# Performance work log

Hardware: AMD Instinct MI355X
Metric: run time of the kernel (lower is better)

The kernel has to match this reference:

```python
import jax, jax.numpy as jnp
import numpy as np

D_MODEL = 1024
N_HEADS = 16
D_HEAD = 64
N_CTX = 2048
ROTARY_DIM = 64
ROTARY_BASE = 10000.0
ATTN_SCALE = 8.0
IGNORE = -100000.0


def _sin_cos(seq_len):
    # rotary_adjacent_pairs=False -> freq repeated as '(2 d)'
    pos = jnp.arange(seq_len, dtype=jnp.float32)
    dim = jnp.arange(ROTARY_DIM // 2, dtype=jnp.float32)
    freq = ROTARY_BASE ** (dim / (ROTARY_DIM / 2))
    freq = jnp.concatenate([freq, freq])  # (2 d)
    angles = pos[:, None] / freq[None, :]  # [S, rotary_dim]
    return jnp.sin(angles), jnp.cos(angles)


def _apply_rotary(x, sin, cos):
    # x: [B, S, H, d_head]; rotary_dim == d_head here, pass-through part is empty
    x_rot = x[..., :ROTARY_DIM]
    x_pass = x[..., ROTARY_DIM:]
    n = ROTARY_DIM // 2
    x_flip = jnp.concatenate([-x_rot[..., n:], x_rot[..., :n]], axis=-1)
    x_rotated = x_rot * cos[None, :, None, :] + x_flip * sin[None, :, None, :]
    return jnp.concatenate([x_rotated, x_pass], axis=-1)


def setup_inputs() -> dict:
    key = jax.random.key(0)
    ks = jax.random.split(key, 12)
    B, S = 1, 2048
    f = lambda k, shp, s=1.0: jax.random.normal(k, shp, dtype=jnp.float32) * s
    return {
        "xq": f(ks[0], (B, S, N_HEADS, D_MODEL)),
        "xk": f(ks[1], (B, S, N_HEADS, D_MODEL)),
        "xv": f(ks[2], (B, S, N_HEADS, D_MODEL)),
        "W_Q": f(ks[3], (N_HEADS, D_MODEL, D_HEAD), 0.02),
        "b_Q": jnp.zeros((N_HEADS, D_HEAD), jnp.float32),
        "W_K": f(ks[4], (N_HEADS, D_MODEL, D_HEAD), 0.02),
        "b_K": jnp.zeros((N_HEADS, D_HEAD), jnp.float32),
        "W_V": f(ks[5], (N_HEADS, D_MODEL, D_HEAD), 0.02),
        "b_V": jnp.zeros((N_HEADS, D_HEAD), jnp.float32),
        "W_O": f(ks[6], (N_HEADS, D_HEAD, D_MODEL), 0.02),
        "b_O": jnp.zeros((D_MODEL,), jnp.float32),
    }


def reference(xq, xk, xv, W_Q, b_Q, W_K, b_K, W_V, b_V, W_O, b_O):
    S = xq.shape[1]
    sin, cos = _sin_cos(S)
    # per-head QKV projections: [B,S,H,dm] x [H,dm,dh] -> [B,S,H,dh]
    q = jnp.einsum('bsnd,nde->bsne', xq, W_Q) + b_Q
    k = jnp.einsum('bsnd,nde->bsne', xk, W_K) + b_K
    v = jnp.einsum('bsnd,nde->bsne', xv, W_V) + b_V
    q = _apply_rotary(q, sin, cos)
    k = _apply_rotary(k, sin, cos)
    # attention scores [B,H,Q,K]
    scores = jnp.einsum('bqne,bkne->bnqk', q, k) / ATTN_SCALE
    causal = jnp.triu(jnp.ones((S, S), dtype=bool), k=1)
    scores = jnp.where(causal[None, None], IGNORE, scores)
    pattern = jax.nn.softmax(scores, axis=-1)
    z = jnp.einsum('bnqk,bkne->bqne', pattern, v)
    # NOTE: faithful to source — head dim is NOT summed; b_O divided by n_heads
    attn_out = jnp.einsum('bqne,ned->bqnd', z, W_O) + b_O / N_HEADS
    return attn_out
```

## Files before the change

### kernel.cpp

```cpp
#include <hip/hip_runtime.h>
#include <hip/hip_bf16.h>
#include <stdint.h>
#include <math.h>

typedef __bf16 bf16_t;
typedef __bf16 bf16x8 __attribute__((ext_vector_type(8)));
typedef __bf16 bf16x4 __attribute__((ext_vector_type(4)));
typedef float  f32x4  __attribute__((ext_vector_type(4)));

#define S_CTX 2048
#define NH    16
#define DM    1024
#define DH    64

#define WS_WT   0
#define WS_WOT  (3*1048576)
#define WS_Q    (4*1048576)
#define WS_K    (WS_Q  + 2097152)
#define WS_VT   (WS_K  + 2097152)
#define WS_Z    (WS_VT + 2097152)

__global__ __launch_bounds__(256) void transpose_w(const float* __restrict__ wq,
                                                   const float* __restrict__ wk,
                                                   const float* __restrict__ wv,
                                                   const float* __restrict__ wo,
                                                   bf16_t* __restrict__ ws) {
  __shared__ bf16_t tl[64 * 68];
  int m = blockIdx.z, h = blockIdx.y, t = blockIdx.x, tid = threadIdx.x;
  const float* in; bf16_t* out; int R, C, r0, c0;
  if (m < 3) { in = (m == 0) ? wq : (m == 1) ? wk : wv; out = ws + m * 1048576;
               R = 1024; C = 64; r0 = t * 64; c0 = 0; }
  else       { in = wo; out = ws + WS_WOT; R = 64; C = 1024; r0 = 0; c0 = t * 64; }
  in  += h * 65536;
  out += h * 65536;
#pragma unroll
  for (int i = 0; i < 4; i++) {
    int idx = tid + i * 256;
    int r = idx >> 4, c = (idx & 15) << 2;
    float4 v = *reinterpret_cast<const float4*>(in + (r0 + r) * C + c0 + c);
    bf16x4 b;
    b[0] = (bf16_t)v.x; b[1] = (bf16_t)v.y; b[2] = (bf16_t)v.z; b[3] = (bf16_t)v.w;
    *reinterpret_cast<bf16x4*>(tl + r * 68 + c) = b;
  }
  __syncthreads();
#pragma unroll
  for (int i = 0; i < 2; i++) {
    int oc = (tid >> 3) + i * 32, ok = (tid & 7) << 3;
    bf16x8 v;
#pragma unroll
    for (int j = 0; j < 8; j++) v[j] = tl[(ok + j) * 68 + oc];
    *reinterpret_cast<bf16x8*>(out + (c0 + oc) * R + r0 + ok) = v;
  }
}

__global__ __launch_bounds__(256) void qkv_proj(const float* __restrict__ xq,
                                                const float* __restrict__ xk,
                                                const float* __restrict__ xv,
                                                const float* __restrict__ bq,
                                                const float* __restrict__ bk,
                                                const float* __restrict__ bv,
                                                bf16_t* __restrict__ ws) {
  __shared__ bf16_t Al[128 * 136];
  __shared__ bf16_t Bl[64 * 136];
  int st = blockIdx.x, h = blockIdx.y, m = blockIdx.z;
  int tid = threadIdx.x, w = tid >> 6, lane = tid & 63, quad = lane >> 4, l15 = lane & 15;
  const float*  in   = (m == 0) ? xq : (m == 1) ? xk : xv;
  const bf16_t* wT   = ws + m * 1048576 + h * 65536;
  const float*  bias = (m == 0) ? bq : (m == 1) ? bk : bv;
  int s0 = st * 128;
  const float* Ab = in + (s0 * 16 + h) * 1024;

  f32x4 acc[2][4];
#pragma unroll
  for (int rt = 0; rt < 2; rt++)
#pragma unroll
    for (int t = 0; t < 4; t++) acc[rt][t] = (f32x4){0.f, 0.f, 0.f, 0.f};

  for (int k0 = 0; k0 < 1024; k0 += 128) {
#pragma unroll
    for (int i = 0; i < 8; i++) {
      int g = tid + i * 256;
      int r = g >> 4, cg = g & 15;
      const float* p = Ab + r * 16384 + k0 + cg * 8;
      float4 v0 = *reinterpret_cast<const float4*>(p);
      float4 v1 = *reinterpret_cast<const float4*>(p + 4);
      bf16x8 b;
      b[0] = (bf16_t)v0.x; b[1] = (bf16_t)v0.y; b[2] = (bf16_t)v0.z; b[3] = (bf16_t)v0.w;
      b[4] = (bf16_t)v1.x; b[5] = (bf16_t)v1.y; b[6] = (bf16_t)v1.z; b[7] = (bf16_t)v1.w;
      *reinterpret_cast<bf16x8*>(Al + r * 136 + cg * 8) = b;
    }
#pragma unroll
    for (int i = 0; i < 4; i++) {
      int g = tid + i * 256;
      int r = g >> 4, cg = g & 15;
      *reinterpret_cast<uint4*>(Bl + r * 136 + cg * 8) =
          *reinterpret_cast<const uint4*>(wT + r * 1024 + k0 + cg * 8);
    }
    __syncthreads();
#pragma unroll
    for (int ks = 0; ks < 4; ks++) {
      bf16x8 a0 = *reinterpret_cast<const bf16x8*>(Al + (w * 32 + l15) * 136 + ks * 32 + quad * 8);
      bf16x8 a1 = *reinterpret_cast<const bf16x8*>(Al + (w * 32 + 16 + l15) * 136 + ks * 32 + quad * 8);
#pragma unroll
      for (int t = 0; t < 4; t++) {
        bf16x8 bb = *reinterpret_cast<const bf16x8*>(Bl + (t * 16 + l15) * 136 + ks * 32 + quad * 8);
        acc[0][t] = __builtin_amdgcn_mfma_f32_16x16x32_bf16(a0, bb, acc[0][t], 0, 0, 0);
        acc[1][t] = __builtin_amdgcn_mfma_f32_16x16x32_bf16(a1, bb, acc[1][t], 0, 0, 0);
      }
    }
    __syncthreads();
  }
#pragma unroll
  for (int t = 0; t < 4; t++) {
    float bval = bias[h * 64 + t * 16 + l15];
#pragma unroll
    for (int rt = 0; rt < 2; rt++)
#pragma unroll
      for (int r = 0; r < 4; r++) acc[rt][t][r] += bval;
  }

  if (m < 2) {
    bf16_t* outp = ws + ((m == 0) ? WS_Q : WS_K) + h * (2048 * 64);
#pragma unroll
    for (int t = 0; t < 2; t++) {
      int c_lo = t * 16 + l15;
      float freq = powf(10000.0f, (float)c_lo * (1.0f / 32.0f));
#pragma unroll
      for (int rt = 0; rt < 2; rt++)
#pragma unroll
        for (int r = 0; r < 4; r++) {
          int s = s0 + w * 32 + rt * 16 + quad * 4 + r;
          float ang = (float)s / freq;
          float sv = sinf(ang), cv = cosf(ang);
          float xl = acc[rt][t][r], xh = acc[rt][t + 2][r];
          acc[rt][t][r]     = xl * cv - xh * sv;
          acc[rt][t + 2][r] = xh * cv + xl * sv;
        }
    }
#pragma unroll
    for (int rt = 0; rt < 2; rt++)
#pragma unroll
      for (int t = 0; t < 4; t++)
#pragma unroll
        for (int r = 0; r < 4; r++) {
          int s = s0 + w * 32 + rt * 16 + quad * 4 + r;
          outp[s * 64 + t * 16 + l15] = (bf16_t)acc[rt][t][r];
        }
  } else {
    bf16_t* outp = ws + WS_VT + h * (64 * 2048);
#pragma unroll
    for (int rt = 0; rt < 2; rt++)
#pragma unroll
      for (int t = 0; t < 4; t++) {
        int e = t * 16 + l15;
        int sbase = s0 + w * 32 + rt * 16 + quad * 4;
        bf16x4 v;
#pragma unroll
        for (int r = 0; r < 4; r++) v[r] = (bf16_t)acc[rt][t][r];
        *reinterpret_cast<bf16x4*>(outp + e * 2048 + sbase) = v;
      }
  }
}

__global__ __launch_bounds__(256) void attn(bf16_t* __restrict__ ws) {
  __shared__ bf16_t Ql[64 * 72];
  __shared__ bf16_t Kl[128 * 72];
  __shared__ bf16_t Vl[64 * 136];
  __shared__ bf16_t Pl[4 * 16 * 136];
  int qt = blockIdx.x, h = blockIdx.y;
  int tid = threadIdx.x, w = tid >> 6, lane = tid & 63, quad = lane >> 4, l15 = lane & 15;
  const bf16_t* qp  = ws + WS_Q  + h * 131072;
  const bf16_t* kp  = ws + WS_K  + h * 131072;
  const bf16_t* vtp = ws + WS_VT + h * 131072;
  bf16_t*       zp  = ws + WS_Z  + h * 131072;
  int s0 = qt * 64;

#pragma unroll
  for (int i = 0; i < 2; i++) {
    int g = tid + i * 256;
    int r = g >> 3, cg = g & 7;
    *reinterpret_cast<uint4*>(Ql + r * 72 + cg * 8) =
        *reinterpret_cast<const uint4*>(qp + (s0 + r) * 64 + cg * 8);
  }

  f32x4 o[4];
#pragma unroll
  for (int t = 0; t < 4; t++) o[t] = (f32x4){0.f, 0.f, 0.f, 0.f};
  float m_i[4], l_i[4];
#pragma unroll
  for (int r = 0; r < 4; r++) { m_i[r] = -__builtin_inff(); l_i[r] = 0.f; }
  bf16_t* Plw = Pl + w * (16 * 136);

  int jmax = qt >> 1;
  for (int j = 0; j <= jmax; j++) {
    __syncthreads();
#pragma unroll
    for (int i = 0; i < 4; i++) {
      int g = tid + i * 256;
      int r = g >> 3, cg = g & 7;
      *reinterpret_cast<uint4*>(Kl + r * 72 + cg * 8) =
          *reinterpret_cast<const uint4*>(kp + (j * 128 + r) * 64 + cg * 8);
    }
#pragma unroll
    for (int i = 0; i < 4; i++) {
      int g = tid + i * 256;
      int r = g >> 4, cg = g & 15;
      *reinterpret_cast<uint4*>(Vl + r * 136 + cg * 8) =
          *reinterpret_cast<const uint4*>(vtp + r * 2048 + j * 128 + cg * 8);
    }
    __syncthreads();

    f32x4 sc[8];
#pragma unroll
    for (int t = 0; t < 8; t++) sc[t] = (f32x4){0.f, 0.f, 0.f, 0.f};
#pragma unroll
    for (int ks = 0; ks < 2; ks++) {
      bf16x8 af = *reinterpret_cast<const bf16x8*>(Ql + (w * 16 + l15) * 72 + ks * 32 + quad * 8);
#pragma unroll
      for (int t = 0; t < 8; t++) {
        bf16x8 bfr = *reinterpret_cast<const bf16x8*>(Kl + (t * 16 + l15) * 72 + ks * 32 + quad * 8);
        sc[t] = __builtin_amdgcn_mfma_f32_16x16x32_bf16(af, bfr, sc[t], 0, 0, 0);
      }
    }
#pragma unroll
    for (int t = 0; t < 8; t++) {
      int kvc = j * 128 + t * 16 + l15;
#pragma unroll
      for (int r = 0; r < 4; r++) {
        int qrow = s0 + w * 16 + quad * 4 + r;
        float sv = sc[t][r] * 0.125f;
        sc[t][r] = (kvc > qrow) ? -1e30f : sv;
      }
    }
    float alpha[4];
#pragma unroll
    for (int r = 0; r < 4; r++) {
      float mx = sc[0][r];
#pragma unroll
      for (int t = 1; t < 8; t++) mx = fmaxf(mx, sc[t][r]);
#pragma unroll
      for (int off = 1; off < 16; off <<= 1) mx = fmaxf(mx, __shfl_xor(mx, off));
      float mn = fmaxf(m_i[r], mx);
      alpha[r] = __expf(m_i[r] - mn);
      float rs = 0.f;
#pragma unroll
      for (int t = 0; t < 8; t++) { sc[t][r] = __expf(sc[t][r] - mn); rs += sc[t][r]; }
#pragma unroll
      for (int off = 1; off < 16; off <<= 1) rs += __shfl_xor(rs, off);
      l_i[r] = l_i[r] * alpha[r] + rs;
      m_i[r] = mn;
    }
#pragma unroll
    for (int t = 0; t < 8; t++)
#pragma unroll
      for (int r = 0; r < 4; r++)
        Plw[(quad * 4 + r) * 136 + t * 16 + l15] = (bf16_t)sc[t][r];
#pragma unroll
    for (int t = 0; t < 4; t++)
#pragma unroll
      for (int r = 0; r < 4; r++) o[t][r] *= alpha[r];
#pragma unroll
    for (int ks = 0; ks < 4; ks++) {
      bf16x8 af = *reinterpret_cast<const bf16x8*>(Plw + l15 * 136 + ks * 32 + quad * 8);
#pragma unroll
      for (int t = 0; t < 4; t++) {
        bf16x8 bfr = *reinterpret_cast<const bf16x8*>(Vl + (t * 16 + l15) * 136 + ks * 32 + quad * 8);
        o[t] = __builtin_amdgcn_mfma_f32_16x16x32_bf16(af, bfr, o[t], 0, 0, 0);
      }
    }
  }
  float inv[4];
#pragma unroll
  for (int r = 0; r < 4; r++) inv[r] = 1.0f / l_i[r];
#pragma unroll
  for (int t = 0; t < 4; t++)
#pragma unroll
    for (int r = 0; r < 4; r++) {
      int s = s0 + w * 16 + quad * 4 + r;
      zp[s * 64 + t * 16 + l15] = (bf16_t)(o[t][r] * inv[r]);
    }
}

__global__ __launch_bounds__(256) void out_proj(const bf16_t* __restrict__ ws,
                                                const float* __restrict__ bo,
                                                float* __restrict__ out) {
  __shared__ bf16_t Zl[128 * 72];
  __shared__ bf16_t Wl[128 * 72];
  int st = blockIdx.x >> 3, dt = blockIdx.x & 7, h = blockIdx.y;
  int tid = threadIdx.x, w = tid >> 6, lane = tid & 63, quad = lane >> 4, l15 = lane & 15;
  int s0 = st * 128, d0 = dt * 128;
  const bf16_t* zp = ws + WS_Z + h * 131072;
  const bf16_t* wo = ws + WS_WOT + h * 65536;
#pragma unroll
  for (int i = 0; i < 4; i++) {
    int g = tid + i * 256;
    int r = g >> 3, cg = g & 7;
    *reinterpret_cast<uint4*>(Zl + r * 72 + cg * 8) =
        *reinterpret_cast<const uint4*>(zp + (s0 + r) * 64 + cg * 8);
  }
#pragma unroll
  for (int i = 0; i < 4; i++) {
    int g = tid + i * 256;
    int r = g >> 3, cg = g & 7;
    *reinterpret_cast<uint4*>(Wl + r * 72 + cg * 8) =
        *reinterpret_cast<const uint4*>(wo + (d0 + r) * 64 + cg * 8);
  }
  __syncthreads();
  f32x4 acc[2][8];
#pragma unroll
  for (int rt = 0; rt < 2; rt++)
#pragma unroll
    for (int t = 0; t < 8; t++) acc[rt][t] = (f32x4){0.f, 0.f, 0.f, 0.f};
#pragma unroll
  for (int ks = 0; ks < 2; ks++) {
    bf16x8 a0 = *reinterpret_cast<const bf16x8*>(Zl + (w * 32 + l15) * 72 + ks * 32 + quad * 8);
    bf16x8 a1 = *reinterpret_cast<const bf16x8*>(Zl + (w * 32 + 16 + l15) * 72 + ks * 32 + quad * 8);
#pragma unroll
    for (int t = 0; t < 8; t++) {
      bf16x8 bb = *reinterpret_cast<const bf16x8*>(Wl + (t * 16 + l15) * 72 + ks * 32 + quad * 8);
      acc[0][t] = __builtin_amdgcn_mfma_f32_16x16x32_bf16(a0, bb, acc[0][t], 0, 0, 0);
      acc[1][t] = __builtin_amdgcn_mfma_f32_16x16x32_bf16(a1, bb, acc[1][t], 0, 0, 0);
    }
  }
#pragma unroll
  for (int t = 0; t < 8; t++) {
    float bval = bo[d0 + t * 16 + l15] * (1.0f / 16.0f);
#pragma unroll
    for (int rt = 0; rt < 2; rt++)
#pragma unroll
      for (int r = 0; r < 4; r++) {
        int s = s0 + w * 32 + rt * 16 + quad * 4 + r;
        out[(s * 16 + h) * 1024 + d0 + t * 16 + l15] = acc[rt][t][r] + bval;
      }
  }
}

extern "C" void kernel_launch(void* const* d_in, const int* in_sizes, int n_in,
                              void* d_out, int out_size, void* d_ws, size_t ws_size,
                              hipStream_t stream) {
  const float* xq = (const float*)d_in[0];
  const float* xk = (const float*)d_in[1];
  const float* xv = (const float*)d_in[2];
  const float* wq = (const float*)d_in[3];
  const float* bq = (const float*)d_in[4];
  const float* wk = (const float*)d_in[5];
  const float* bk = (const float*)d_in[6];
  const float* wv = (const float*)d_in[7];
  const float* bv = (const float*)d_in[8];
  const float* wo = (const float*)d_in[9];
  const float* bo = (const float*)d_in[10];
  bf16_t* ws  = (bf16_t*)d_ws;
  float*  out = (float*)d_out;

  hipLaunchKernelGGL(transpose_w, dim3(16, 16, 4), dim3(256), 0, stream, wq, wk, wv, wo, ws);
  hipLaunchKernelGGL(qkv_proj,    dim3(16, 16, 3), dim3(256), 0, stream, xq, xk, xv, bq, bk, bv, ws);
  hipLaunchKernelGGL(attn,        dim3(32, 16),    dim3(256), 0, stream, ws);
  hipLaunchKernelGGL(out_proj,    dim3(128, 16),   dim3(256), 0, stream, ws, bo, out);
}
```

Measured before the change: 567.6 us.

## Load QKV projection tiles via global_load_lds with XOR-swizzled LDS layout

Replaces the register-staged fp32 loads (with bf16 conversion before the LDS write) in the QKV projection with direct global-to-LDS 16-byte async loads. A tile stays fp32 in LDS and is converted to bf16 when read for the MFMA. An XOR swizzle replaces row padding to avoid bank conflicts, and the K-tile shrinks from 128 to 64 to fit the larger fp32 tile. This removes VGPR staging and conversion from the load path, but doubles the loop iterations and barriers and adds conversion work on the LDS reads.

```diff
diff --git a/kernel.cpp b/kernel.cpp
--- a/kernel.cpp
+++ b/kernel.cpp
@@ -19,6 +19,12 @@
 #define WS_K    (WS_Q  + 2097152)
 #define WS_VT   (WS_K  + 2097152)
 #define WS_Z    (WS_VT + 2097152)
+
+__device__ __forceinline__ void async16(void* lds, const void* g) {
+  __builtin_amdgcn_global_load_lds(
+      (const __attribute__((address_space(1))) unsigned int*)g,
+      (__attribute__((address_space(3))) unsigned int*)lds, 16, 0, 0);
+}
 
 __global__ __launch_bounds__(256) void transpose_w(const float* __restrict__ wq,
                                                    const float* __restrict__ wk,
@@ -60,8 +66,8 @@
                                                 const float* __restrict__ bk,
                                                 const float* __restrict__ bv,
                                                 bf16_t* __restrict__ ws) {
-  __shared__ bf16_t Al[128 * 136];
-  __shared__ bf16_t Bl[64 * 136];
+  __shared__ __attribute__((aligned(16))) float  Al[128 * 64];
+  __shared__ __attribute__((aligned(16))) bf16_t Bl[64 * 64];
   int st = blockIdx.x, h = blockIdx.y, m = blockIdx.z;
   int tid = threadIdx.x, w = tid >> 6, lane = tid & 63, quad = lane >> 4, l15 = lane & 15;
   const float*  in   = (m == 0) ? xq : (m == 1) ? xk : xv;
@@ -70,40 +76,54 @@
   int s0 = st * 128;
   const float* Ab = in + (s0 * 16 + h) * 1024;
 
+  int a_r = lane >> 4;
+  int a_j = lane & 15;
+  int b_r = lane >> 3;
+  int b_j = lane & 7;
+
   f32x4 acc[2][4];
 #pragma unroll
   for (int rt = 0; rt < 2; rt++)
 #pragma unroll
     for (int t = 0; t < 4; t++) acc[rt][t] = (f32x4){0.f, 0.f, 0.f, 0.f};
 
-  for (int k0 = 0; k0 < 1024; k0 += 128) {
+  for (int k0 = 0; k0 < 1024; k0 += 64) {
 #pragma unroll
     for (int i = 0; i < 8; i++) {
-      int g = tid + i * 256;
-      int r = g >> 4, cg = g & 15;
-      const float* p = Ab + r * 16384 + k0 + cg * 8;
-      float4 v0 = *reinterpret_cast<const float4*>(p);
-      float4 v1 = *reinterpret_cast<const float4*>(p + 4);
-      bf16x8 b;
-      b[0] = (bf16_t)v0.x; b[1] = (bf16_t)v0.y; b[2] = (bf16_t)v0.z; b[3] = (bf16_t)v0.w;
-      b[4] = (bf16_t)v1.x; b[5] = (bf16_t)v1.y; b[6] = (bf16_t)v1.z; b[7] = (bf16_t)v1.w;
-      *reinterpret_cast<bf16x8*>(Al + r * 136 + cg * 8) = b;
-    }
-#pragma unroll
-    for (int i = 0; i < 4; i++) {
-      int g = tid + i * 256;
-      int r = g >> 4, cg = g & 15;
-      *reinterpret_cast<uint4*>(Bl + r * 136 + cg * 8) =
-          *reinterpret_cast<const uint4*>(wT + r * 1024 + k0 + cg * 8);
+      int g = w * 8 + i;
+      int r = g * 4 + a_r;
+      int c = a_j ^ (r & 15);
+      async16(Al + g * 256, Ab + r * 16384 + k0 + c * 4);
+    }
+#pragma unroll
+    for (int i = 0; i < 2; i++) {
+      int g = w * 2 + i;
+      int r = g * 8 + b_r;
+      int c = b_j ^ (r & 7);
+      async16(Bl + g * 512, wT + r * 1024 + k0 + c * 8);
     }
     __syncthreads();
 #pragma unroll
-    for (int ks = 0; ks < 4; ks++) {
-      bf16x8 a0 = *reinterpret_cast<const bf16x8*>(Al + (w * 32 + l15) * 136 + ks * 32 + quad * 8);
-      bf16x8 a1 = *reinterpret_cast<const bf16x8*>(Al + (w * 32 + 16 + l15) * 136 + ks * 32 + quad * 8);
+    for (int ks = 0; ks < 2; ks++) {
+      int cA0 = ((ks * 8 + quad * 2) ^ l15) << 2;
+      int cA1 = cA0 ^ 4;
+      const float* Ar0 = Al + (w * 32 + l15) * 64;
+      const float* Ar1 = Ar0 + 16 * 64;
+      f32x4 lo0 = *reinterpret_cast<const f32x4*>(Ar0 + cA0);
+      f32x4 hi0 = *reinterpret_cast<const f32x4*>(Ar0 + cA1);
+      f32x4 lo1 = *reinterpret_cast<const f32x4*>(Ar1 + cA0);
+      f32x4 hi1 = *reinterpret_cast<const f32x4*>(Ar1 + cA1);
+      bf16x8 a0, a1;
+#pragma unroll
+      for (int jj = 0; jj < 4; jj++) {
+        a0[jj] = (bf16_t)lo0[jj]; a0[jj + 4] = (bf16_t)hi0[jj];
+        a1[jj] = (bf16_t)lo1[jj]; a1[jj + 4] = (bf16_t)hi1[jj];
+      }
 #pragma unroll
       for (int t = 0; t < 4; t++) {
-        bf16x8 bb = *reinterpret_cast<const bf16x8*>(Bl + (t * 16 + l15) * 136 + ks * 32 + quad * 8);
+        int rB = t * 16 + l15;
+        bf16x8 bb = *reinterpret_cast<const bf16x8*>(
+            Bl + rB * 64 + (((ks * 4 + quad) ^ (l15 & 7)) << 3));
         acc[0][t] = __builtin_amdgcn_mfma_f32_16x16x32_bf16(a0, bb, acc[0][t], 0, 0, 0);
         acc[1][t] = __builtin_amdgcn_mfma_f32_16x16x32_bf16(a1, bb, acc[1][t], 0, 0, 0);
       }
```

New measurement: 530.1 us. 1.07x faster.

## Double-buffer QKV projection with async global-to-LDS loads and swizzled layout

Applied to the files above, without the earlier changes.

The QKV projection kernel now stages fp32 activations and bf16 weights directly into LDS with global_load_lds in 32-wide K chunks, double-buffered so the next chunk loads while the current one is computed. The fp32-to-bf16 conversion moves from the store path to the LDS read path, and an XOR swizzle replaces row padding to avoid bank conflicts. Launch bounds request 4 blocks per CU and LDS use shrinks, which should raise occupancy. In exchange, the loop has more barriers per K step, relies on hand-written vmcnt waits, and fetches fp32 rather than bf16 into LDS.

```diff
diff --git a/kernel.cpp b/kernel.cpp
--- a/kernel.cpp
+++ b/kernel.cpp
@@ -19,6 +19,12 @@
 #define WS_K    (WS_Q  + 2097152)
 #define WS_VT   (WS_K  + 2097152)
 #define WS_Z    (WS_VT + 2097152)
+
+__device__ __forceinline__ void async16(void* lds, const void* g) {
+  __builtin_amdgcn_global_load_lds(
+      (const __attribute__((address_space(1))) unsigned int*)g,
+      (__attribute__((address_space(3))) unsigned int*)lds, 16, 0, 0);
+}
 
 __global__ __launch_bounds__(256) void transpose_w(const float* __restrict__ wq,
                                                    const float* __restrict__ wk,
@@ -53,15 +59,15 @@
   }
 }
 
-__global__ __launch_bounds__(256) void qkv_proj(const float* __restrict__ xq,
-                                                const float* __restrict__ xk,
-                                                const float* __restrict__ xv,
-                                                const float* __restrict__ bq,
-                                                const float* __restrict__ bk,
-                                                const float* __restrict__ bv,
-                                                bf16_t* __restrict__ ws) {
-  __shared__ bf16_t Al[128 * 136];
-  __shared__ bf16_t Bl[64 * 136];
+__global__ __launch_bounds__(256, 4) void qkv_proj(const float* __restrict__ xq,
+                                                   const float* __restrict__ xk,
+                                                   const float* __restrict__ xv,
+                                                   const float* __restrict__ bq,
+                                                   const float* __restrict__ bk,
+                                                   const float* __restrict__ bv,
+                                                   bf16_t* __restrict__ ws) {
+  __shared__ __attribute__((aligned(16))) float  Al[2 * 128 * 32];
+  __shared__ __attribute__((aligned(16))) bf16_t Bl[2 * 64 * 32];
   int st = blockIdx.x, h = blockIdx.y, m = blockIdx.z;
   int tid = threadIdx.x, w = tid >> 6, lane = tid & 63, quad = lane >> 4, l15 = lane & 15;
   const float*  in   = (m == 0) ? xq : (m == 1) ? xk : xv;
@@ -70,46 +76,67 @@
   int s0 = st * 128;
   const float* Ab = in + (s0 * 16 + h) * 1024;
 
+  int a_r = lane >> 3;
+  int a_c = (lane & 7) ^ a_r;
+  int b_r = lane >> 2;
+  int b_c = (lane & 3) ^ ((lane >> 3) & 3);
+
   f32x4 acc[2][4];
 #pragma unroll
   for (int rt = 0; rt < 2; rt++)
 #pragma unroll
     for (int t = 0; t < 4; t++) acc[rt][t] = (f32x4){0.f, 0.f, 0.f, 0.f};
 
-  for (int k0 = 0; k0 < 1024; k0 += 128) {
-#pragma unroll
-    for (int i = 0; i < 8; i++) {
-      int g = tid + i * 256;
-      int r = g >> 4, cg = g & 15;
-      const float* p = Ab + r * 16384 + k0 + cg * 8;
-      float4 v0 = *reinterpret_cast<const float4*>(p);
-      float4 v1 = *reinterpret_cast<const float4*>(p + 4);
-      bf16x8 b;
-      b[0] = (bf16_t)v0.x; b[1] = (bf16_t)v0.y; b[2] = (bf16_t)v0.z; b[3] = (bf16_t)v0.w;
-      b[4] = (bf16_t)v1.x; b[5] = (bf16_t)v1.y; b[6] = (bf16_t)v1.z; b[7] = (bf16_t)v1.w;
-      *reinterpret_cast<bf16x8*>(Al + r * 136 + cg * 8) = b;
-    }
+  auto stage = [&](int buf, int k0) {
+    float*  Ad = Al + buf * 4096;
+    bf16_t* Bd = Bl + buf * 2048;
 #pragma unroll
     for (int i = 0; i < 4; i++) {
-      int g = tid + i * 256;
-      int r = g >> 4, cg = g & 15;
-      *reinterpret_cast<uint4*>(Bl + r * 136 + cg * 8) =
-          *reinterpret_cast<const uint4*>(wT + r * 1024 + k0 + cg * 8);
-    }
-    __syncthreads();
-#pragma unroll
-    for (int ks = 0; ks < 4; ks++) {
-      bf16x8 a0 = *reinterpret_cast<const bf16x8*>(Al + (w * 32 + l15) * 136 + ks * 32 + quad * 8);
-      bf16x8 a1 = *reinterpret_cast<const bf16x8*>(Al + (w * 32 + 16 + l15) * 136 + ks * 32 + quad * 8);
-#pragma unroll
-      for (int t = 0; t < 4; t++) {
-        bf16x8 bb = *reinterpret_cast<const bf16x8*>(Bl + (t * 16 + l15) * 136 + ks * 32 + quad * 8);
-        acc[0][t] = __builtin_amdgcn_mfma_f32_16x16x32_bf16(a0, bb, acc[0][t], 0, 0, 0);
-        acc[1][t] = __builtin_amdgcn_mfma_f32_16x16x32_bf16(a1, bb, acc[1][t], 0, 0, 0);
-      }
-    }
-    __syncthreads();
-  }
+      int g = w * 4 + i;
+      async16(Ad + g * 256, Ab + (g * 8 + a_r) * 16384 + k0 + a_c * 4);
+    }
+    async16(Bd + w * 512, wT + (w * 16 + b_r) * 1024 + k0 + b_c * 8);
+  };
+
+  auto compute = [&](int buf) {
+    const float*  Ac = Al + buf * 4096;
+    const bf16_t* Bc = Bl + buf * 2048;
+    int ca = ((quad * 2) ^ (l15 & 7)) << 2;
+    const float* Ar0 = Ac + (w * 32 + l15) * 32;
+    const float* Ar1 = Ar0 + 16 * 32;
+    f32x4 lo0 = *reinterpret_cast<const f32x4*>(Ar0 + ca);
+    f32x4 hi0 = *reinterpret_cast<const f32x4*>(Ar0 + (ca ^ 4));
+    f32x4 lo1 = *reinterpret_cast<const f32x4*>(Ar1 + ca);
+    f32x4 hi1 = *reinterpret_cast<const f32x4*>(Ar1 + (ca ^ 4));
+    bf16x8 a0, a1;
+#pragma unroll
+    for (int jj = 0; jj < 4; jj++) {
+      a0[jj] = (bf16_t)lo0[jj]; a0[jj + 4] = (bf16_t)hi0[jj];
+      a1[jj] = (bf16_t)lo1[jj]; a1[jj + 4] = (bf16_t)hi1[jj];
+    }
+    int cb = (quad ^ ((l15 >> 1) & 3)) << 3;
+#pragma unroll
+    for (int t = 0; t < 4; t++) {
+      bf16x8 bb = *reinterpret_cast<const bf16x8*>(Bc + (t * 16 + l15) * 32 + cb);
+      acc[0][t] = __builtin_amdgcn_mfma_f32_16x16x32_bf16(a0, bb, acc[0][t], 0, 0, 0);
+      acc[1][t] = __builtin_amdgcn_mfma_f32_16x16x32_bf16(a1, bb, acc[1][t], 0, 0, 0);
+    }
+  };
+
+  stage(0, 0);
+  int cur = 0;
+  for (int k0 = 0; k0 < 1024 - 32; k0 += 32) {
+    stage(cur ^ 1, k0 + 32);
+    asm volatile("s_waitcnt vmcnt(5)" ::: "memory");
+    __builtin_amdgcn_s_barrier();
+    compute(cur);
+    __builtin_amdgcn_s_barrier();
+    cur ^= 1;
+  }
+  asm volatile("s_waitcnt vmcnt(0)" ::: "memory");
+  __builtin_amdgcn_s_barrier();
+  compute(cur);
+
 #pragma unroll
   for (int t = 0; t < 4; t++) {
     float bval = bias[h * 64 + t * 16 + l15];
```

Result: faster. 524.5 us (-7.6%).
